# Performance work log

Hardware: AMD Instinct MI355X
Metric: run time of the kernel (lower is better)

The kernel has to match this reference:

```python
import jax, jax.numpy as jnp
import numpy as np

LAYER_BS = 63
N_SITES = 12
B = 2048


def _kaiming_uniform(key, shape, fan_in):
    # torch kaiming_uniform_ with a=0: bound = sqrt(6/fan_in)
    bound = np.sqrt(6.0 / fan_in)
    return jax.random.uniform(key, shape, jnp.float32, -bound, bound)


def _cnn12(x, w):
    # x: (B, L, 12, Cin); w: (L, 3*Cin, Cout)
    nn0 = jnp.roll(x, -1, axis=-2) + jnp.roll(x, 3, axis=-2)
    nnn0 = jnp.roll(x, -2, axis=-2) + jnp.roll(x, 4, axis=-2)
    c0 = jnp.concatenate([nn0, nnn0], axis=-1)          # (B,L,12,2*Cin)
    c1 = c0 + jnp.roll(c0, -2, axis=-2)
    allc = jnp.concatenate([x, c1], axis=-1)            # (B,L,12,3*Cin)
    return jnp.einsum('blsc,lco->blso', allc, w)


def _batch_linear(x, w, b):
    # x: (B, L, F); w: (L, F, O); b: (L, O)
    return jnp.einsum('blf,lfo->blo', x, w) + b


def setup_inputs() -> dict:
    key = jax.random.key(0)
    ks = jax.random.split(key, 9)
    zs = jax.random.normal(ks[0], (B, LAYER_BS, N_SITES, 2), jnp.float32)
    # CNN weights: (L, 3*Cin, Cout); kaiming fan_in = 3*Cin
    w1 = _kaiming_uniform(ks[1], (LAYER_BS, 6, 32), 6)
    w2 = _kaiming_uniform(ks[2], (LAYER_BS, 96, 64), 96)
    fw1 = _kaiming_uniform(ks[3], (LAYER_BS, 128, 64), 128)
    fb1 = jax.random.uniform(ks[4], (LAYER_BS, 64), jnp.float32, -1 / np.sqrt(128), 1 / np.sqrt(128))
    fw2 = _kaiming_uniform(ks[5], (LAYER_BS, 64, 64), 64)
    fb2 = jax.random.uniform(ks[6], (LAYER_BS, 64), jnp.float32, -1 / np.sqrt(64), 1 / np.sqrt(64))
    fw3 = _kaiming_uniform(ks[7], (LAYER_BS, 64, 1), 64)
    fb3 = jax.random.uniform(ks[8], (LAYER_BS, 1), jnp.float32, -1 / np.sqrt(64), 1 / np.sqrt(64))
    return {"zs": zs, "w1": w1, "w2": w2, "fw1": fw1, "fb1": fb1,
            "fw2": fw2, "fb2": fb2, "fw3": fw3, "fb3": fb3}


def reference(zs, w1, w2, fw1, fb1, fw2, fb2, fw3, fb3):
    h = jax.nn.relu(_cnn12(zs, w1))                     # (B,L,12,32)
    h = jax.nn.relu(_cnn12(h, w2))                      # (B,L,12,64)
    h = jnp.concatenate([h.mean(axis=-2), h.max(axis=-2)], axis=-1)
    h = jax.nn.relu(_batch_linear(h, fw1, fb1))
    h = jax.nn.relu(_batch_linear(h, fw2, fb2))
    out = _batch_linear(h, fw3, fb3)                    # (B,L,1)
    return out[..., 0]                                  # (B,L)
```

## Files before the change

### kernel.cpp

```cpp
#include <hip/hip_runtime.h>


#define LNUM 63
#define BT 16
#define NBT 128
#define WSL 19968

typedef __attribute__((ext_vector_type(8))) _Float16 half8;
typedef __attribute__((ext_vector_type(2))) _Float16 half2v;
typedef __attribute__((ext_vector_type(4))) float floatx4;
typedef __attribute__((ext_vector_type(4))) unsigned uint4v;

static __device__ __forceinline__ unsigned cvtpk(float a, float b) {
    return __builtin_bit_cast(unsigned, __builtin_amdgcn_cvt_pkrtz(a, b));
}
static __device__ __forceinline__ half2v u2h(unsigned u) { return __builtin_bit_cast(half2v, u); }
static __device__ __forceinline__ unsigned h2u(half2v h) { return __builtin_bit_cast(unsigned, h); }
static __device__ __forceinline__ half2v hmax2(half2v a, half2v b) {
    half2v r;
    r[0] = a[0] > b[0] ? a[0] : b[0];
    r[1] = a[1] > b[1] ? a[1] : b[1];
    return r;
}
static __device__ __forceinline__ float hlo16(unsigned short s) {
    return (float)__builtin_bit_cast(_Float16, s);
}
static __device__ __forceinline__ int w12(int v) { return v >= 12 ? v - 12 : v; }
static __device__ __forceinline__ float2 add2(float2 a, float2 b) { return make_float2(a.x + b.x, a.y + b.y); }

#define O_POOL  13056
#define O_POOL2 15232
#define O_G2    16384

__global__ void prep(const float* __restrict__ w2, const float* __restrict__ fw1,
                     const float* __restrict__ fw2, unsigned short* __restrict__ ws) {
    const int l = blockIdx.x, t = threadIdx.x;
    const int o = t & 63, g = t >> 6;
    unsigned* w2t = (unsigned*)(ws + (size_t)l * WSL);
    const float* w2l = w2 + (size_t)l * 6144;
    #pragma unroll
    for (int i = 0; i < 12; ++i) {
        int cp = g + 4 * i, c = 2 * cp;
        w2t[o * 52 + cp] = cvtpk(w2l[c * 64 + o], w2l[(c + 1) * 64 + o]);
    }
    unsigned* f1t = (unsigned*)(ws + (size_t)l * WSL + 6656);
    const float* f1l = fw1 + (size_t)l * 8192;
    #pragma unroll
    for (int i = 0; i < 16; ++i) {
        int cp = g + 4 * i, c = 2 * cp;
        f1t[o * 68 + cp] = cvtpk(f1l[c * 64 + o], f1l[(c + 1) * 64 + o]);
    }
    unsigned* f2t = (unsigned*)(ws + (size_t)l * WSL + 15360);
    const float* f2l = fw2 + (size_t)l * 4096;
    #pragma unroll
    for (int i = 0; i < 8; ++i) {
        int cp = g + 4 * i, c = 2 * cp;
        f2t[o * 36 + cp] = cvtpk(f2l[c * 64 + o], f2l[(c + 1) * 64 + o]);
    }
}

__global__ __launch_bounds__(256, 4) void fused_nn(
    const float* __restrict__ zs,  const float* __restrict__ w1,
    const float* __restrict__ fb1, const float* __restrict__ fb2,
    const float* __restrict__ fw3, const float* __restrict__ fb3,
    const unsigned short* __restrict__ ws,
    float* __restrict__ out)
{
    __shared__ __align__(16) unsigned short U[18432];
    __shared__ __align__(16) float s_w1[192];
    __shared__ __align__(16) float s_x[BT * 24];
    __shared__ __align__(16) float s_fw3[64];

    const int t    = threadIdx.x;
    const int lane = t & 63;
    const int wv   = t >> 6;
    const int n    = lane & 15;
    const int quad = lane >> 4;
    const int l    = blockIdx.x / NBT;
    const int b0   = (blockIdx.x % NBT) * BT;

    if (t < 96) {
        int b = t / 6, q = t - 6 * b;
        float4 f = *(const float4*)(zs + ((size_t)(b0 + b) * LNUM + l) * 24 + q * 4);
        *(float4*)(s_x + b * 24 + q * 4) = f;
    }
    if (t < 48) ((float4*)s_w1)[t] = ((const float4*)(w1 + (size_t)l * 192))[t];
    if (t >= 96 && t < 112) ((float4*)s_fw3)[t - 96] = ((const float4*)(fw3 + (size_t)l * 64))[t - 96];
    __syncthreads();

    {
        const int b = t >> 4, cpair = t & 15, c0 = cpair * 2;
        const float* xb = s_x + b * 24;
        float2 xv[12], xr[12], xA[12], xB[12];
        #pragma unroll
        for (int s = 0; s < 12; ++s) xv[s] = *(const float2*)(xb + 2 * s);
        #pragma unroll
        for (int s = 0; s < 12; ++s) xr[s] = add2(xv[w12(s + 1)], xv[w12(s + 11)]);
        #pragma unroll
        for (int s = 0; s < 12; ++s) {
            xA[s] = add2(xr[w12(s + 2)], xr[w12(s + 10)]);
            xB[s] = add2(xr[w12(s + 3)], xr[w12(s + 9)]);
        }
        const float2 w0 = *(const float2*)(s_w1 + c0);
        const float2 w1v = *(const float2*)(s_w1 + 32 + c0);
        const float2 w2v = *(const float2*)(s_w1 + 64 + c0);
        const float2 w3v = *(const float2*)(s_w1 + 96 + c0);
        const float2 w4v = *(const float2*)(s_w1 + 128 + c0);
        const float2 w5v = *(const float2*)(s_w1 + 160 + c0);
        unsigned hp[12];
        #pragma unroll
        for (int s = 0; s < 12; ++s) {
            float hx = xv[s].x*w0.x + xv[s].y*w1v.x + xA[s].x*w2v.x + xA[s].y*w3v.x
                     + xB[s].x*w4v.x + xB[s].y*w5v.x;
            float hy = xv[s].x*w0.y + xv[s].y*w1v.y + xA[s].x*w2v.y + xA[s].y*w3v.y
                     + xB[s].x*w4v.y + xB[s].y*w5v.y;
            hp[s] = cvtpk(fmaxf(hx, 0.f), fmaxf(hy, 0.f));
        }
        half2v hh[12], hr[12];
        #pragma unroll
        for (int s = 0; s < 12; ++s) hh[s] = u2h(hp[s]);
        #pragma unroll
        for (int s = 0; s < 12; ++s) hr[s] = hh[w12(s + 1)] + hh[w12(s + 11)];
        unsigned* dwU = (unsigned*)U;
        const int g = cpair >> 2, jj = cpair & 3;
        #pragma unroll
        for (int s = 0; s < 12; ++s) {
            half2v hA = hr[w12(s + 2)] + hr[w12(s + 10)];
            half2v hB = hr[w12(s + 3)] + hr[w12(s + 9)];
            const int row = b * 12 + s;
            const int base = row * 48 + ((g ^ (s & 3)) << 2) + jj;
            dwU[base]      = hp[s];
            dwU[base + 16] = h2u(hA);
            dwU[base + 32] = h2u(hB);
        }
    }
    __syncthreads();

    floatx4 acc[3][4];
    #pragma unroll
    for (int mi = 0; mi < 3; ++mi)
        #pragma unroll
        for (int nt = 0; nt < 4; ++nt) acc[mi][nt] = (floatx4){0.f, 0.f, 0.f, 0.f};
    {
        half8 af[3][3];
        const int sw = (quad ^ (n & 3)) * 8;
        #pragma unroll
        for (int mi = 0; mi < 3; ++mi) {
            const int row = (3 * wv + mi) * 16 + n;
            #pragma unroll
            for (int ks = 0; ks < 3; ++ks)
                af[mi][ks] = *(const half8*)(U + row * 96 + ks * 32 + sw);
        }
        const uint4v* w2q = (const uint4v*)(ws + (size_t)l * WSL);
        #pragma unroll
        for (int ks = 0; ks < 3; ++ks) {
            uint4v bw[4];
            #pragma unroll
            for (int nt = 0; nt < 4; ++nt)
                bw[nt] = w2q[(nt * 16 + n) * 13 + ks * 4 + quad];
            #pragma unroll
            for (int mi = 0; mi < 3; ++mi)
                #pragma unroll
                for (int nt = 0; nt < 4; ++nt)
                    acc[mi][nt] = __builtin_amdgcn_mfma_f32_16x16x32_f16(
                        af[mi][ks], __builtin_bit_cast(half8, bw[nt]), acc[mi][nt], 0, 0, 0);
        }
    }
    __syncthreads();

    #pragma unroll
    for (int mi = 0; mi < 3; ++mi) {
        const int r0 = (3 * wv + mi) * 16 + quad * 4;
        #pragma unroll
        for (int nt = 0; nt < 4; ++nt) {
            const int o = nt * 16 + n;
            unsigned* dst = (unsigned*)U + o * 101 + (r0 >> 1);
            dst[0] = cvtpk(fmaxf(acc[mi][nt][0], 0.f), fmaxf(acc[mi][nt][1], 0.f));
            dst[1] = cvtpk(fmaxf(acc[mi][nt][2], 0.f), fmaxf(acc[mi][nt][3], 0.f));
        }
    }
    __syncthreads();

    {
        const int o = lane;
        #pragma unroll
        for (int bb = 0; bb < 4; ++bb) {
            const int b = wv * 4 + bb;
            const half2v* src = (const half2v*)(U + o * 202 + b * 12);
            half2v v0 = src[0];
            half2v sm = v0, mx = v0;
            #pragma unroll
            for (int j = 1; j < 6; ++j) {
                half2v v = src[j];
                sm = sm + v;
                mx = hmax2(mx, v);
            }
            float s = (float)sm[0] + (float)sm[1];
            float m = fmaxf((float)mx[0], (float)mx[1]);
            unsigned pk = cvtpk(s * (1.f / 12.f), m);
            U[O_POOL + b * 136 + o]      = (unsigned short)(pk & 0xffffu);
            U[O_POOL + b * 136 + 64 + o] = (unsigned short)(pk >> 16);
        }
    }
    __syncthreads();

    {
        const int o = wv * 16 + n;
        const float bias = fb1[(size_t)l * 64 + o];
        floatx4 a1 = (floatx4){bias, bias, bias, bias};
        const uint4v* f1q = (const uint4v*)(ws + (size_t)l * WSL + 6656);
        #pragma unroll
        for (int ks = 0; ks < 4; ++ks) {
            half8 av = *(const half8*)(U + O_POOL + n * 136 + ks * 32 + quad * 8);
            uint4v bw = f1q[o * 17 + ks * 4 + quad];
            a1 = __builtin_amdgcn_mfma_f32_16x16x32_f16(av, __builtin_bit_cast(half8, bw), a1, 0, 0, 0);
        }
        #pragma unroll
        for (int i = 0; i < 2; ++i) {
            unsigned pk = cvtpk(fmaxf(a1[2 * i], 0.f), fmaxf(a1[2 * i + 1], 0.f));
            U[O_POOL2 + (quad * 4 + 2 * i)     * 72 + o] = (unsigned short)(pk & 0xffffu);
            U[O_POOL2 + (quad * 4 + 2 * i + 1) * 72 + o] = (unsigned short)(pk >> 16);
        }
    }
    __syncthreads();

    {
        const int o = wv * 16 + n;
        const float bias = fb2[(size_t)l * 64 + o];
        floatx4 a2 = (floatx4){bias, bias, bias, bias};
        const uint4v* f2q = (const uint4v*)(ws + (size_t)l * WSL + 15360);
        #pragma unroll
        for (int ks = 0; ks < 2; ++ks) {
            half8 av = *(const half8*)(U + O_POOL2 + n * 72 + ks * 32 + quad * 8);
            uint4v bw = f2q[o * 9 + ks * 4 + quad];
            a2 = __builtin_amdgcn_mfma_f32_16x16x32_f16(av, __builtin_bit_cast(half8, bw), a2, 0, 0, 0);
        }
        #pragma unroll
        for (int i = 0; i < 2; ++i) {
            unsigned pk = cvtpk(fmaxf(a2[2 * i], 0.f), fmaxf(a2[2 * i + 1], 0.f));
            U[O_G2 + (quad * 4 + 2 * i)     * 72 + o] = (unsigned short)(pk & 0xffffu);
            U[O_G2 + (quad * 4 + 2 * i + 1) * 72 + o] = (unsigned short)(pk >> 16);
        }
    }
    __syncthreads();

    if (t < 16) {
        float a = fb3[l];
        const unsigned short* g2r = U + O_G2 + t * 72;
        #pragma unroll
        for (int c = 0; c < 64; ++c) a += hlo16(g2r[c]) * s_fw3[c];
        out[(size_t)(b0 + t) * LNUM + l] = a;
    }
}

extern "C" void kernel_launch(void* const* d_in, const int* in_sizes, int n_in,
                              void* d_out, int out_size, void* d_ws, size_t ws_size,
                              hipStream_t stream) {
    const float* zs  = (const float*)d_in[0];
    const float* w1  = (const float*)d_in[1];
    const float* w2  = (const float*)d_in[2];
    const float* fw1 = (const float*)d_in[3];
    const float* fb1 = (const float*)d_in[4];
    const float* fw2 = (const float*)d_in[5];
    const float* fb2 = (const float*)d_in[6];
    const float* fw3 = (const float*)d_in[7];
    const float* fb3 = (const float*)d_in[8];
    float* out = (float*)d_out;
    unsigned short* ws = (unsigned short*)d_ws;

    hipLaunchKernelGGL(prep, dim3(LNUM), dim3(256), 0, stream, w2, fw1, fw2, ws);
    hipLaunchKernelGGL(fused_nn, dim3(LNUM * NBT), dim3(256), 0, stream,
                       zs, w1, fb1, fb2, fw3, fb3, ws, out);
}
```

Measured before the change: 138.4 us.

## Repack LDS layouts, drop staging buffers, split prep grid, vectorize pooling

Removes the shared-memory staging of zs, w1 and fw3 and the barrier after it; each thread now reads its inputs straight from global memory. The second-conv output is repacked with a new row stride and per-batch layout so it can be written and read with 64-bit LDS accesses. The pooled mean/max is stored as one packed word, with fw1 pre-permuted to match. Pool2 now aliases the start of U, which needs an extra barrier inside the FC1 stage. The prep kernel is split across a 2-D grid to give it more parallelism. Risks are redundant global loads of zs and w1 across threads, plus the extra barrier.

```diff
diff --git a/kernel.cpp b/kernel.cpp
--- a/kernel.cpp
+++ b/kernel.cpp
@@ -28,34 +28,38 @@
 static __device__ __forceinline__ int w12(int v) { return v >= 12 ? v - 12 : v; }
 static __device__ __forceinline__ float2 add2(float2 a, float2 b) { return make_float2(a.x + b.x, a.y + b.y); }
 
-#define O_POOL  13056
-#define O_POOL2 15232
-#define O_G2    16384
+#define H2S    130
+#define O_POOL 16640
+#define O_POOL2 0
+#define O_G2   1280
 
 __global__ void prep(const float* __restrict__ w2, const float* __restrict__ fw1,
                      const float* __restrict__ fw2, unsigned short* __restrict__ ws) {
     const int l = blockIdx.x, t = threadIdx.x;
     const int o = t & 63, g = t >> 6;
-    unsigned* w2t = (unsigned*)(ws + (size_t)l * WSL);
-    const float* w2l = w2 + (size_t)l * 6144;
-    #pragma unroll
-    for (int i = 0; i < 12; ++i) {
-        int cp = g + 4 * i, c = 2 * cp;
-        w2t[o * 52 + cp] = cvtpk(w2l[c * 64 + o], w2l[(c + 1) * 64 + o]);
-    }
-    unsigned* f1t = (unsigned*)(ws + (size_t)l * WSL + 6656);
-    const float* f1l = fw1 + (size_t)l * 8192;
-    #pragma unroll
-    for (int i = 0; i < 16; ++i) {
-        int cp = g + 4 * i, c = 2 * cp;
-        f1t[o * 68 + cp] = cvtpk(f1l[c * 64 + o], f1l[(c + 1) * 64 + o]);
-    }
-    unsigned* f2t = (unsigned*)(ws + (size_t)l * WSL + 15360);
-    const float* f2l = fw2 + (size_t)l * 4096;
-    #pragma unroll
-    for (int i = 0; i < 8; ++i) {
-        int cp = g + 4 * i, c = 2 * cp;
-        f2t[o * 36 + cp] = cvtpk(f2l[c * 64 + o], f2l[(c + 1) * 64 + o]);
+    if (blockIdx.y == 0) {
+        unsigned* w2t = (unsigned*)(ws + (size_t)l * WSL);
+        const float* w2l = w2 + (size_t)l * 6144;
+        #pragma unroll
+        for (int i = 0; i < 12; ++i) {
+            int cp = g + 4 * i, c = 2 * cp;
+            w2t[o * 52 + cp] = cvtpk(w2l[c * 64 + o], w2l[(c + 1) * 64 + o]);
+        }
+    } else {
+        unsigned* f1t = (unsigned*)(ws + (size_t)l * WSL + 6656);
+        const float* f1l = fw1 + (size_t)l * 8192;
+        #pragma unroll
+        for (int i = 0; i < 16; ++i) {
+            int cp = g + 4 * i;
+            f1t[o * 68 + cp] = cvtpk(f1l[cp * 64 + o], f1l[(64 + cp) * 64 + o]);
+        }
+        unsigned* f2t = (unsigned*)(ws + (size_t)l * WSL + 15360);
+        const float* f2l = fw2 + (size_t)l * 4096;
+        #pragma unroll
+        for (int i = 0; i < 8; ++i) {
+            int cp = g + 4 * i, c = 2 * cp;
+            f2t[o * 36 + cp] = cvtpk(f2l[c * 64 + o], f2l[(c + 1) * 64 + o]);
+        }
     }
 }
 
@@ -66,10 +70,7 @@
     const unsigned short* __restrict__ ws,
     float* __restrict__ out)
 {
-    __shared__ __align__(16) unsigned short U[18432];
-    __shared__ __align__(16) float s_w1[192];
-    __shared__ __align__(16) float s_x[BT * 24];
-    __shared__ __align__(16) float s_fw3[64];
+    __shared__ __align__(16) unsigned short U[18816];
 
     const int t    = threadIdx.x;
     const int lane = t & 63;
@@ -79,21 +80,17 @@
     const int l    = blockIdx.x / NBT;
     const int b0   = (blockIdx.x % NBT) * BT;
 
-    if (t < 96) {
-        int b = t / 6, q = t - 6 * b;
-        float4 f = *(const float4*)(zs + ((size_t)(b0 + b) * LNUM + l) * 24 + q * 4);
-        *(float4*)(s_x + b * 24 + q * 4) = f;
-    }
-    if (t < 48) ((float4*)s_w1)[t] = ((const float4*)(w1 + (size_t)l * 192))[t];
-    if (t >= 96 && t < 112) ((float4*)s_fw3)[t - 96] = ((const float4*)(fw3 + (size_t)l * 64))[t - 96];
-    __syncthreads();
-
     {
         const int b = t >> 4, cpair = t & 15, c0 = cpair * 2;
-        const float* xb = s_x + b * 24;
+        const float* xb = zs + ((size_t)(b0 + b) * LNUM + l) * 24;
+        float4 xq[6];
+        #pragma unroll
+        for (int q = 0; q < 6; ++q) xq[q] = *(const float4*)(xb + q * 4);
         float2 xv[12], xr[12], xA[12], xB[12];
         #pragma unroll
-        for (int s = 0; s < 12; ++s) xv[s] = *(const float2*)(xb + 2 * s);
+        for (int s = 0; s < 12; ++s)
+            xv[s] = (s & 1) ? make_float2(xq[s >> 1].z, xq[s >> 1].w)
+                            : make_float2(xq[s >> 1].x, xq[s >> 1].y);
         #pragma unroll
         for (int s = 0; s < 12; ++s) xr[s] = add2(xv[w12(s + 1)], xv[w12(s + 11)]);
         #pragma unroll
@@ -101,12 +98,13 @@
             xA[s] = add2(xr[w12(s + 2)], xr[w12(s + 10)]);
             xB[s] = add2(xr[w12(s + 3)], xr[w12(s + 9)]);
         }
-        const float2 w0 = *(const float2*)(s_w1 + c0);
-        const float2 w1v = *(const float2*)(s_w1 + 32 + c0);
-        const float2 w2v = *(const float2*)(s_w1 + 64 + c0);
-        const float2 w3v = *(const float2*)(s_w1 + 96 + c0);
-        const float2 w4v = *(const float2*)(s_w1 + 128 + c0);
-        const float2 w5v = *(const float2*)(s_w1 + 160 + c0);
+        const float* wl = w1 + (size_t)l * 192 + c0;
+        const float2 w0  = *(const float2*)(wl);
+        const float2 w1v = *(const float2*)(wl + 32);
+        const float2 w2v = *(const float2*)(wl + 64);
+        const float2 w3v = *(const float2*)(wl + 96);
+        const float2 w4v = *(const float2*)(wl + 128);
+        const float2 w5v = *(const float2*)(wl + 160);
         unsigned hp[12];
         #pragma unroll
         for (int s = 0; s < 12; ++s) {
@@ -170,13 +168,17 @@
 
     #pragma unroll
     for (int mi = 0; mi < 3; ++mi) {
-        const int r0 = (3 * wv + mi) * 16 + quad * 4;
+        const int r0g  = (3 * wv + mi) * 16 + quad * 4;
+        const int bidx = r0g / 12;
+        const int s0   = r0g - bidx * 12;
+        const int dbase = bidx * 8 + (s0 >> 1);
         #pragma unroll
         for (int nt = 0; nt < 4; ++nt) {
             const int o = nt * 16 + n;
-            unsigned* dst = (unsigned*)U + o * 101 + (r0 >> 1);
-            dst[0] = cvtpk(fmaxf(acc[mi][nt][0], 0.f), fmaxf(acc[mi][nt][1], 0.f));
-            dst[1] = cvtpk(fmaxf(acc[mi][nt][2], 0.f), fmaxf(acc[mi][nt][3], 0.f));
+            uint2 v;
+            v.x = cvtpk(fmaxf(acc[mi][nt][0], 0.f), fmaxf(acc[mi][nt][1], 0.f));
+            v.y = cvtpk(fmaxf(acc[mi][nt][2], 0.f), fmaxf(acc[mi][nt][3], 0.f));
+            *(uint2*)((unsigned*)U + o * H2S + dbase) = v;
         }
     }
     __syncthreads();
@@ -186,20 +188,17 @@
         #pragma unroll
         for (int bb = 0; bb < 4; ++bb) {
             const int b = wv * 4 + bb;
-            const half2v* src = (const half2v*)(U + o * 202 + b * 12);
-            half2v v0 = src[0];
-            half2v sm = v0, mx = v0;
-            #pragma unroll
-            for (int j = 1; j < 6; ++j) {
-                half2v v = src[j];
-                sm = sm + v;
-                mx = hmax2(mx, v);
-            }
+            const unsigned* src = (const unsigned*)U + o * H2S + b * 8;
+            uint2 p0 = *(const uint2*)(src);
+            uint2 p1 = *(const uint2*)(src + 2);
+            uint2 p2 = *(const uint2*)(src + 4);
+            half2v v0 = u2h(p0.x), v1 = u2h(p0.y), v2 = u2h(p1.x);
+            half2v v3 = u2h(p1.y), v4 = u2h(p2.x), v5 = u2h(p2.y);
+            half2v sm = ((v0 + v1) + (v2 + v3)) + (v4 + v5);
+            half2v mx = hmax2(hmax2(hmax2(v0, v1), hmax2(v2, v3)), hmax2(v4, v5));
             float s = (float)sm[0] + (float)sm[1];
             float m = fmaxf((float)mx[0], (float)mx[1]);
-            unsigned pk = cvtpk(s * (1.f / 12.f), m);
-            U[O_POOL + b * 136 + o]      = (unsigned short)(pk & 0xffffu);
-            U[O_POOL + b * 136 + 64 + o] = (unsigned short)(pk >> 16);
+            ((unsigned*)U)[O_POOL / 2 + b * 68 + o] = cvtpk(s * (1.f / 12.f), m);
         }
     }
     __syncthreads();
@@ -215,6 +214,7 @@
             uint4v bw = f1q[o * 17 + ks * 4 + quad];
             a1 = __builtin_amdgcn_mfma_f32_16x16x32_f16(av, __builtin_bit_cast(half8, bw), a1, 0, 0, 0);
         }
+        __syncthreads();
         #pragma unroll
         for (int i = 0; i < 2; ++i) {
             unsigned pk = cvtpk(fmaxf(a1[2 * i], 0.f), fmaxf(a1[2 * i + 1], 0.f));
@@ -246,9 +246,16 @@
 
     if (t < 16) {
         float a = fb3[l];
-        const unsigned short* g2r = U + O_G2 + t * 72;
-        #pragma unroll
-        for (int c = 0; c < 64; ++c) a += hlo16(g2r[c]) * s_fw3[c];
+        const float* w3 = fw3 + (size_t)l * 64;
+        #pragma unroll
+        for (int c4 = 0; c4 < 16; ++c4) {
+            uint2 u2 = *(const uint2*)(U + O_G2 + t * 72 + c4 * 4);
+            float4 w = *(const float4*)(w3 + c4 * 4);
+            a += hlo16((unsigned short)(u2.x & 0xffff)) * w.x
+               + hlo16((unsigned short)(u2.x >> 16))    * w.y
+               + hlo16((unsigned short)(u2.y & 0xffff)) * w.z
+               + hlo16((unsigned short)(u2.y >> 16))    * w.w;
+        }
         out[(size_t)(b0 + t) * LNUM + l] = a;
     }
 }
@@ -268,7 +275,7 @@
     float* out = (float*)d_out;
     unsigned short* ws = (unsigned short*)d_ws;
 
-    hipLaunchKernelGGL(prep, dim3(LNUM), dim3(256), 0, stream, w2, fw1, fw2, ws);
+    hipLaunchKernelGGL(prep, dim3(LNUM, 2), dim3(256), 0, stream, w2, fw1, fw2, ws);
     hipLaunchKernelGGL(fused_nn, dim3(LNUM * NBT), dim3(256), 0, stream,
                        zs, w1, fb1, fb2, fw3, fb3, ws, out);
 }
```

New measurement: 137.3 us. No clear change (-0.8%).
